# Performance work log

Hardware: AMD Instinct MI355X
Metric: run time of the kernel (lower is better)

The kernel has to match this reference:

```python
import jax, jax.numpy as jnp
import numpy as np

IN_CH = 256
OUT_CH = 256
STATE = 384
OUT_SEQ = 32
B_SZ = 8
SEQ = 512


def setup_inputs() -> dict:
    key = jax.random.key(0)
    ks = jax.random.split(key, 8)
    rmin, rmax, max_phase = 0.0, 1.0, 6.283
    u1 = jax.random.uniform(ks[0], (STATE,))
    u2 = jax.random.uniform(ks[1], (STATE,))
    # standard LRU stable-ring initialization
    nu_log = jnp.log(-0.5 * jnp.log(u1 * (rmax + rmin) * (rmax - rmin) + rmin ** 2))
    theta_log = jnp.log(max_phase * u2)
    lam_mod = jnp.exp(-jnp.exp(nu_log))
    gamma_log = jnp.log(jnp.sqrt(1.0 - lam_mod ** 2))
    B_re = jax.random.normal(ks[2], (STATE, IN_CH)) / np.sqrt(2 * IN_CH)
    B_im = jax.random.normal(ks[3], (STATE, IN_CH)) / np.sqrt(2 * IN_CH)
    C_re = jax.random.normal(ks[4], (OUT_CH, STATE)) / np.sqrt(STATE)
    C_im = jax.random.normal(ks[5], (OUT_CH, STATE)) / np.sqrt(STATE)
    D = jax.random.normal(ks[6], (OUT_CH, IN_CH)) / np.sqrt(IN_CH)
    x = jax.random.normal(ks[7], (B_SZ, SEQ, IN_CH))
    return dict(x=x, nu_log=nu_log, theta_log=theta_log, gamma_log=gamma_log,
                B_re=B_re, B_im=B_im, C_re=C_re, C_im=C_im, D=D)


def _lru(x, h_re, h_im, nu_log, theta_log, gamma_log, B_re, B_im, C_re, C_im, D):
    """One LRU pass over a full sequence. x: [B,S,C]. h_*: [B,N] initial complex state.
    Diagonal complex recurrence h_t = Lambda*h_{t-1} + gamma*(B x_t); y_t = Re(C h_t) + D x_t."""
    lam_mod = jnp.exp(-jnp.exp(nu_log))              # |Lambda| in (0,1)
    lre = lam_mod * jnp.cos(jnp.exp(theta_log))      # [N]
    lim = lam_mod * jnp.sin(jnp.exp(theta_log))
    gamma = jnp.exp(gamma_log)
    # input projection for whole sequence (complex, split into re/im)
    u_re = gamma * jnp.einsum('bsc,nc->bsn', x, B_re)  # [B,S,N]
    u_im = gamma * jnp.einsum('bsc,nc->bsn', x, B_im)

    def step(h, u):
        hre, him = h
        ur, ui = u
        nre = lre * hre - lim * him + ur
        nim = lre * him + lim * hre + ui
        return (nre, nim), (nre, nim)

    (h_re, h_im), (hs_re, hs_im) = jax.lax.scan(
        step, (h_re, h_im),
        (jnp.swapaxes(u_re, 0, 1), jnp.swapaxes(u_im, 0, 1)))  # scan over S
    hs_re = jnp.swapaxes(hs_re, 0, 1)  # [B,S,N]
    hs_im = jnp.swapaxes(hs_im, 0, 1)
    y = (jnp.einsum('bsn,on->bso', hs_re, C_re)
         - jnp.einsum('bsn,on->bso', hs_im, C_im)
         + jnp.einsum('bsc,oc->bso', x, D))
    return y, h_re, h_im


def reference(x, nu_log, theta_log, gamma_log, B_re, B_im, C_re, C_im, D):
    bsz = x.shape[0]
    h_re = jnp.zeros((bsz, STATE), x.dtype)   # state=None on first call -> zeros
    h_im = jnp.zeros((bsz, STATE), x.dtype)
    outs = []
    for _ in range(OUT_SEQ):
        x, h_re, h_im = _lru(x, h_re, h_im, nu_log, theta_log, gamma_log,
                             B_re, B_im, C_re, C_im, D)
        outs.append(x[:, -1:])
    return jnp.concatenate(outs, axis=-2)  # [B, OUT_SEQ, OUT_CH]
```

## Files before the change

### kernel.cpp

```cpp
#include <hip/hip_runtime.h>
#include <hip/hip_bf16.h>
#include <math.h>

typedef unsigned short u16;
typedef __attribute__((ext_vector_type(8))) short bf16x8;
typedef __attribute__((ext_vector_type(4))) float f32x4;
typedef __attribute__((ext_vector_type(16))) float f32x16;

#define IN_CH   256
#define STATE   384
#define OUT_SEQ 32
#define B_SZ    8
#define SEQ     512
#define M_ROWS  4096
#define NJ      768

#define PS_WB  (NJ*IN_CH)
#define PS_WC  (IN_CH*NJ)
#define PS_WD  (IN_CH*IN_CH)
#define PS_Z   ((size_t)M_ROWS*NJ)
#define PS_X   ((size_t)M_ROWS*IN_CH)

static constexpr size_t B_U   = 0;
static constexpr size_t B_Z   = B_U  + 8*(size_t)M_ROWS*IN_CH*4;
static constexpr size_t B_XA  = B_Z  + 3*(size_t)M_ROWS*NJ*2;
static constexpr size_t B_XB  = B_XA + 3*(size_t)M_ROWS*IN_CH*2;
static constexpr size_t B_WB  = B_XB + 3*(size_t)M_ROWS*IN_CH*2;
static constexpr size_t B_WC  = B_WB + 3*(size_t)PS_WB*2;
static constexpr size_t B_WD  = B_WC + 3*(size_t)PS_WC*2;
static constexpr size_t B_LAM = B_WD + 3*(size_t)PS_WD*2;
static constexpr size_t B_HC  = B_LAM + 2*768*4;

__device__ __forceinline__ u16 f2b(float v) {
    __hip_bfloat16 h = __float2bfloat16(v);
    return *(u16*)&h;
}
__device__ __forceinline__ float b2f(u16 u) {
    __hip_bfloat16 h = *(__hip_bfloat16*)&u;
    return __bfloat162float(h);
}
__device__ __forceinline__ void split3(float v, u16& a, u16& b, u16& c) {
    a = f2b(v);  float r1 = v  - b2f(a);
    b = f2b(r1); float r2 = r1 - b2f(b);
    c = f2b(r2);
}

__device__ __forceinline__ size_t a_idx(int row, int k, int NKC) {
    return ((size_t)(((row >> 5)*NKC + (k >> 5))*2 + ((k >> 4) & 1))*2 + ((k >> 3) & 1))*256
           + (size_t)(row & 31)*8 + (k & 7);
}

__device__ __forceinline__ void frag_decode(int r, int& t32, int& h, int& hi5,
                                            int& lo5, int& e) {
    t32 = r >> 10; int r2 = r & 1023;
    h = r2 >> 9;   int r3 = r2 & 511;
    hi5 = r3 >> 8; int r4 = r3 & 255;
    lo5 = r4 >> 3; e = r4 & 7;
}

__global__ void prep_lam_hc(const float* __restrict__ nu_log,
                            const float* __restrict__ th_log,
                            float* __restrict__ lam, float* __restrict__ lam16,
                            float* __restrict__ hc0) {
    int n = threadIdx.x;
    if (n < STATE) {
        float lm = expf(-expf(nu_log[n]));
        float th = expf(th_log[n]);
        float ar = lm * cosf(th), ai = lm * sinf(th);
        lam[2*n] = ar; lam[2*n+1] = ai;
        float pr = ar, pi = ai;
#pragma unroll
        for (int i = 0; i < 4; ++i) {
            float nr = pr*pr - pi*pi, ni = 2.f*pr*pi;
            pr = nr; pi = ni;
        }
        lam16[2*n] = pr; lam16[2*n+1] = pi;
    }
    for (int i = threadIdx.x; i < B_SZ*NJ; i += blockDim.x) hc0[i] = 0.f;
}

__global__ void prep_wb(const float* __restrict__ B_re, const float* __restrict__ B_im,
                        const float* __restrict__ gamma_log, u16* __restrict__ W) {
    int idx = blockIdx.x*blockDim.x + threadIdx.x;
    int c32 = idx >> 13, r = idx & 8191;
    int t32,h,hi5,lo5,e; frag_decode(r, t32,h,hi5,lo5,e);
    int j = c32*32 + lo5;
    int k = t32*32 + (2*h + hi5)*8 + e;
    int n = j >> 1;
    float g = expf(gamma_log[n]);
    float v = g * ((j & 1) ? B_im[n*IN_CH + k] : B_re[n*IN_CH + k]);
    u16 a,b,cc; split3(v,a,b,cc);
    W[idx] = a; W[idx + PS_WB] = b; W[idx + 2*PS_WB] = cc;
}

__global__ void prep_wcd(const float* __restrict__ C_re, const float* __restrict__ C_im,
                         const float* __restrict__ D,
                         u16* __restrict__ WC, u16* __restrict__ WD) {
    int idx = blockIdx.x*blockDim.x + threadIdx.x;
    if (idx < PS_WC) {
        int c32 = idx / 24576, r = idx % 24576;
        int t32,h,hi5,lo5,e; frag_decode(r, t32,h,hi5,lo5,e);
        int o = c32*32 + lo5;
        int j = t32*32 + (2*h + hi5)*8 + e;
        int n = j >> 1;
        float v = (j & 1) ? -C_im[o*STATE + n] : C_re[o*STATE + n];
        u16 a,b,c; split3(v,a,b,c);
        WC[idx] = a; WC[idx + PS_WC] = b; WC[idx + 2*PS_WC] = c;
    } else {
        int q = idx - PS_WC;
        int c32 = q >> 13, r = q & 8191;
        int t32,h,hi5,lo5,e; frag_decode(r, t32,h,hi5,lo5,e);
        int o = c32*32 + lo5;
        int c = t32*32 + (2*h + hi5)*8 + e;
        float v = D[o*IN_CH + c];
        u16 a,b,cc; split3(v,a,b,cc);
        WD[q] = a; WD[q + PS_WD] = b; WD[q + 2*PS_WD] = cc;
    }
}

__global__ void prep_x(const float* __restrict__ x,
                       u16* __restrict__ X1, u16* __restrict__ X2, u16* __restrict__ X3) {
    int idx = blockIdx.x*blockDim.x + threadIdx.x;
    int row = idx >> 8, k = idx & 255;
    u16 a,b,c; split3(x[idx],a,b,c);
    size_t o = a_idx(row, k, 8);
    X1[o] = a; X2[o] = b; X3[o] = c;
}

__device__ __constant__ const int cPI[6] = {0,0,1,0,1,2};
__device__ __constant__ const int cPJ[6] = {0,1,0,2,1,0};

struct G1P { const u16* A[3]; };

__global__ __launch_bounds__(512, 2)
void front_k(G1P ga, const u16* __restrict__ WBp, const u16* __restrict__ WDp,
             u16* __restrict__ Z1, u16* __restrict__ Z2, u16* __restrict__ Z3,
             float* __restrict__ P,
             const float* __restrict__ lam, const float* __restrict__ lam16,
             const float2* __restrict__ HcIn, float2* __restrict__ HcOut) {
    __shared__ __align__(16) float Ls[512*34];
    __shared__ float2 car[32][16];
    __shared__ float2 hp[32][16];
    const int tid = threadIdx.x, lane = tid & 63, w = tid >> 6;
    const int l15 = lane & 15, q = lane >> 4;
    const int hb = q >> 1, hi5q = q & 1;
    const int hi5 = lane >> 5, lo5 = lane & 31;

    if (blockIdx.x >= 192) {
        const int mt = blockIdx.x - 192;
        const int wr = w & 1, wc = w >> 1;
        const int m32 = mt*2 + wr;
        f32x16 acc[2];
#pragma unroll
        for (int cj = 0; cj < 2; ++cj)
#pragma unroll
            for (int i = 0; i < 16; ++i) acc[cj][i] = 0.f;

        bf16x8 av[2][3][2], bv[2][2][3][2];
        auto loadA = [&](int buf, int kc) {
#pragma unroll
            for (int p = 0; p < 3; ++p)
#pragma unroll
                for (int h = 0; h < 2; ++h)
                    av[buf][p][h] = *(const bf16x8*)(ga.A[p]
                        + ((((size_t)(m32*8 + kc)*2 + h)*2 + hi5) << 8) + lo5*8);
        };
        auto loadB = [&](int buf, int kc) {
#pragma unroll
            for (int cj = 0; cj < 2; ++cj)
#pragma unroll
                for (int p = 0; p < 3; ++p)
#pragma unroll
                    for (int h = 0; h < 2; ++h)
                        bv[buf][cj][p][h] = *(const bf16x8*)(WDp + (size_t)p*PS_WD
                            + ((((size_t)((wc*2 + cj)*8 + kc)*2 + h)*2 + hi5) << 8) + lo5*8);
        };
        loadA(0, 0); loadB(0, 0);
        loadA(1, 1); loadB(1, 1);
#pragma unroll
        for (int kc = 0; kc < 8; ++kc) {
            const int cb = kc & 1;
#pragma unroll
            for (int t6 = 0; t6 < 6; ++t6)
#pragma unroll
                for (int cj = 0; cj < 2; ++cj)
#pragma unroll
                    for (int h = 0; h < 2; ++h)
                        acc[cj] = __builtin_amdgcn_mfma_f32_32x32x16_bf16(
                            av[cb][cPI[t6]][h], bv[cb][cj][cPJ[t6]][h], acc[cj], 0, 0, 0);
            if (kc + 2 < 8) { loadA(cb, kc + 2); loadB(cb, kc + 2); }
        }
#pragma unroll
        for (int cj = 0; cj < 2; ++cj)
#pragma unroll
            for (int reg = 0; reg < 16; ++reg) {
                int row = mt*64 + wr*32 + (reg & 3) + 8*(reg >> 2) + 4*hi5;
                int col = wc*64 + cj*32 + lo5;
                P[(size_t)row*IN_CH + col] = acc[cj][reg];
            }
        return;
    }

    const int b = blockIdx.x & 7, jt = blockIdx.x >> 3;

    f32x4 acc[4][2];
#pragma unroll
    for (int i = 0; i < 4; ++i)
#pragma unroll
        for (int n16 = 0; n16 < 2; ++n16) acc[i][n16] = 0.f;

    bf16x8 av[2][4][3], bv[2][2][3];
    auto loadA = [&](int buf, int kc) {
#pragma unroll
        for (int p = 0; p < 3; ++p)
#pragma unroll
            for (int i = 0; i < 4; ++i) {
                int m16 = i*8 + w;
                int row32 = b*16 + (m16 >> 1);
                int rin = ((m16 & 1) << 4) + l15;
                av[buf][i][p] = *(const bf16x8*)(ga.A[p]
                    + ((((size_t)(row32*8 + kc)*2 + hb)*2 + hi5q) << 8) + rin*8);
            }
    };
    auto loadB = [&](int buf, int kc) {
#pragma unroll
        for (int p = 0; p < 3; ++p)
#pragma unroll
            for (int n16 = 0; n16 < 2; ++n16)
                bv[buf][n16][p] = *(const bf16x8*)(WBp + (size_t)p*PS_WB
                    + ((((size_t)(jt*8 + kc)*2 + hb)*2 + hi5q) << 8) + (n16*16 + l15)*8);
    };

    loadA(0, 0); loadB(0, 0);
    loadA(1, 1); loadB(1, 1);
#pragma unroll
    for (int kc = 0; kc < 8; ++kc) {
        const int cb = kc & 1;
#pragma unroll
        for (int t6 = 0; t6 < 6; ++t6)
#pragma unroll
            for (int i = 0; i < 4; ++i)
#pragma unroll
                for (int n16 = 0; n16 < 2; ++n16)
                    acc[i][n16] = __builtin_amdgcn_mfma_f32_16x16x32_bf16(
                        av[cb][i][cPI[t6]], bv[cb][n16][cPJ[t6]], acc[i][n16], 0, 0, 0);
        if (kc + 2 < 8) { loadA(cb, kc + 2); loadB(cb, kc + 2); }
    }

#pragma unroll
    for (int i = 0; i < 4; ++i) {
        int m16 = i*8 + w;
#pragma unroll
        for (int n16 = 0; n16 < 2; ++n16)
#pragma unroll
            for (int r = 0; r < 4; ++r) {
                int s = m16*16 + q*4 + r;
                int jl = n16*16 + l15;
                Ls[s*34 + jl] = acc[i][n16][r];
            }
    }
    __syncthreads();

    {
        int st = tid & 15, ch = tid >> 4;
        int n = jt*16 + st;
        float lre = lam[2*n], lim = lam[2*n+1];
        float hr = 0.f, hm = 0.f;
#pragma unroll
        for (int t = 0; t < 16; ++t) {
            int s = ch*16 + t;
            float2 u = *(const float2*)&Ls[s*34 + 2*st];
            float nr = fmaf(lre, hr, fmaf(-lim, hm, u.x));
            float nm = fmaf(lre, hm, fmaf( lim, hr, u.y));
            hr = nr; hm = nm;
        }
        car[ch][st] = make_float2(hr, hm);
    }
    __syncthreads();

    {
        int st2 = 2*w + hi5, ch2 = lane & 31;
        int n = jt*16 + st2;
        float2 e = car[ch2][st2];
        float Ar = lam16[2*n], Ai = lam16[2*n+1];
        float Br = e.x, Bi = e.y;
#pragma unroll
        for (int d = 1; d < 32; d <<= 1) {
            int src = (lane & 32) | ((lane - d) & 31);
            float pAr = __shfl(Ar, src), pAi = __shfl(Ai, src);
            float pBr = __shfl(Br, src), pBi = __shfl(Bi, src);
            if (ch2 >= d) {
                float nAr = Ar*pAr - Ai*pAi;
                float nAi = Ar*pAi + Ai*pAr;
                float nBr = fmaf(Ar, pBr, fmaf(-Ai, pBi, Br));
                float nBi = fmaf(Ar, pBi, fmaf( Ai, pBr, Bi));
                Ar = nAr; Ai = nAi; Br = nBr; Bi = nBi;
            }
        }
        float2 s0 = HcIn[(size_t)b*STATE + n];
        if (ch2 == 31) {
            float fr = fmaf(Ar, s0.x, fmaf(-Ai, s0.y, Br));
            float fi = fmaf(Ar, s0.y, fmaf( Ai, s0.x, Bi));
            HcOut[(size_t)b*STATE + n] = make_float2(fr, fi);
        }
        int srcp = (lane & 32) | ((lane - 1) & 31);
        float eAr = __shfl(Ar, srcp), eAi = __shfl(Ai, srcp);
        float eBr = __shfl(Br, srcp), eBi = __shfl(Bi, srcp);
        float sr, si;
        if (ch2 == 0) { sr = s0.x; si = s0.y; }
        else {
            sr = fmaf(eAr, s0.x, fmaf(-eAi, s0.y, eBr));
            si = fmaf(eAr, s0.y, fmaf( eAi, s0.x, eBi));
        }
        hp[ch2][st2] = make_float2(sr, si);
    }
    __syncthreads();

    {
        int st = tid & 15, ch = tid >> 4;
        int n = jt*16 + st;
        float lre = lam[2*n], lim = lam[2*n+1];
        float2 hh = hp[ch][st];
        int j0 = jt*32 + 2*st;
#pragma unroll
        for (int t = 0; t < 16; ++t) {
            int s = ch*16 + t;
            float2 u = *(const float2*)&Ls[s*34 + 2*st];
            float nr = fmaf(lre, hh.x, fmaf(-lim, hh.y, u.x));
            float ni = fmaf(lre, hh.y, fmaf( lim, hh.x, u.y));
            hh.x = nr; hh.y = ni;
            u16 a1,a2,a3, c1,c2,c3;
            split3(nr, a1,a2,a3);
            split3(ni, c1,c2,c3);
            size_t zo = a_idx(b*512 + s, j0, 24);
            ushort2 t2;
            t2.x = a1; t2.y = c1; *(ushort2*)(Z1 + zo) = t2;
            t2.x = a2; t2.y = c2; *(ushort2*)(Z2 + zo) = t2;
            t2.x = a3; t2.y = c3; *(ushort2*)(Z3 + zo) = t2;
        }
    }
}

struct G2P {
    const u16* Z[3]; const u16* WC; const float* P;
    u16* O1; u16* O2; u16* O3; float* outp; int iter;
};

__global__ __launch_bounds__(512, 2)
void gemm2_k(G2P g) {
    __shared__ __align__(16) float Lred[64*64];
    const int tid = threadIdx.x, lane = tid & 63, w = tid >> 6;
    const int kg = w >> 2, wq = w & 3;
    const int wr = wq & 1, wcq = wq >> 1;
    const int m0 = blockIdx.x*64, n0 = blockIdx.y*64;
    const int hi5 = lane >> 5, lo5 = lane & 31;
    const int c32 = (n0 >> 5) + wcq;
    const int m32 = blockIdx.x*2 + wr;
    const int cbase = kg*12;

    f32x16 accv;
#pragma unroll
    for (int i = 0; i < 16; ++i) accv[i] = 0.f;

    auto aptr = [&](int p, int c, int h) -> const u16* {
        return g.Z[p] + ((((size_t)(m32*24 + c)*2 + h)*2 + hi5) << 8) + lo5*8;
    };
    auto bptr = [&](int p, int c, int h) -> const u16* {
        return g.WC + (size_t)p*PS_WC
               + ((((size_t)(c32*24 + c)*2 + h)*2 + hi5) << 8) + lo5*8;
    };

    bf16x8 bwin[3][4][2];
    auto loadB = [&](int wnd, int tlo, int thi) {
#pragma unroll
        for (int p = 0; p < 3; ++p)
#pragma unroll
            for (int t = 0; t < 4; ++t) {
                if (t < tlo || t >= thi) continue;
#pragma unroll
                for (int h = 0; h < 2; ++h)
                    bwin[p][t][h] = *(const bf16x8*)bptr(p, cbase + wnd*4 + t, h);
            }
    };
    bf16x8 av[2][3][2];
    auto loadA = [&](int buf, int t) {
#pragma unroll
        for (int p = 0; p < 3; ++p)
#pragma unroll
            for (int h = 0; h < 2; ++h)
                av[buf][p][h] = *(const bf16x8*)aptr(p, cbase + t, h);
    };

    loadA(0, 0);
    loadB(0, 0, 4);
    loadA(1, 1);
#pragma unroll
    for (int t = 0; t < 12; ++t) {
        if ((t & 3) == 2 && t < 8) loadB((t >> 2) + 1, 0, 2);
        const int cb = t & 1;
        const int tw = t & 3;
#pragma unroll
        for (int t6 = 0; t6 < 6; ++t6)
            accv = __builtin_amdgcn_mfma_f32_32x32x16_bf16(
                av[cb][cPI[t6]][0], bwin[cPJ[t6]][tw][0],
                __builtin_amdgcn_mfma_f32_32x32x16_bf16(
                    av[cb][cPI[t6]][1], bwin[cPJ[t6]][tw][1], accv, 0, 0, 0),
                0, 0, 0);
        if ((t & 3) == 3 && t < 8) loadB((t >> 2) + 1, 2, 4);
        if (t + 2 < 12) loadA(cb, t + 2);
    }

    if (kg == 1) {
#pragma unroll
        for (int reg = 0; reg < 16; ++reg) {
            int rl = wr*32 + (reg & 3) + 8*(reg >> 2) + 4*hi5;
            int cl = wcq*32 + lo5;
            Lred[rl*64 + cl] = accv[reg];
        }
    }
    __syncthreads();
    if (kg == 0) {
#pragma unroll
        for (int reg = 0; reg < 16; ++reg) {
            int rl = wr*32 + (reg & 3) + 8*(reg >> 2) + 4*hi5;
            int cl = wcq*32 + lo5;
            int row = m0 + rl, col = n0 + cl;
            float v = accv[reg] + Lred[rl*64 + cl] + g.P[(size_t)row*IN_CH + col];
            u16 a,b,c; split3(v, a,b,c);
            size_t o = a_idx(row, col, 8);
            g.O1[o] = a; g.O2[o] = b; g.O3[o] = c;
            if ((row & (SEQ-1)) == SEQ-1)
                g.outp[(size_t)((row >> 9)*OUT_SEQ + g.iter)*IN_CH + col] = v;
        }
    }
}

extern "C" void kernel_launch(void* const* d_in, const int* in_sizes, int n_in,
                              void* d_out, int out_size, void* d_ws, size_t ws_size,
                              hipStream_t stream) {
    const float* x_in      = (const float*)d_in[0];
    const float* nu_log    = (const float*)d_in[1];
    const float* theta_log = (const float*)d_in[2];
    const float* gamma_log = (const float*)d_in[3];
    const float* B_re      = (const float*)d_in[4];
    const float* B_im      = (const float*)d_in[5];
    const float* C_re      = (const float*)d_in[6];
    const float* C_im      = (const float*)d_in[7];
    const float* D         = (const float*)d_in[8];
    float* out = (float*)d_out;

    char* ws = (char*)d_ws;
    float* P = (float*)(ws + B_U);
    u16* Z1 = (u16*)(ws + B_Z);
    u16* Z2 = Z1 + PS_Z;
    u16* Z3 = Z2 + PS_Z;
    u16* XA1 = (u16*)(ws + B_XA);
    u16* XA2 = XA1 + PS_X;
    u16* XA3 = XA2 + PS_X;
    u16* XB1 = (u16*)(ws + B_XB);
    u16* XB2 = XB1 + PS_X;
    u16* XB3 = XB2 + PS_X;
    u16* WB  = (u16*)(ws + B_WB);
    u16* WCt = (u16*)(ws + B_WC);
    u16* WDt = (u16*)(ws + B_WD);
    float* lam   = (float*)(ws + B_LAM);
    float* lam16 = lam + 768;
    float2* Hc0  = (float2*)(ws + B_HC);
    float2* Hc1  = Hc0 + (size_t)B_SZ*STATE;

    prep_lam_hc<<<1, 384, 0, stream>>>(nu_log, theta_log, lam, lam16, (float*)Hc0);
    prep_wb<<<PS_WB/256, 256, 0, stream>>>(B_re, B_im, gamma_log, WB);
    prep_wcd<<<(PS_WC + PS_WD)/256, 256, 0, stream>>>(C_re, C_im, D, WCt, WDt);
    prep_x<<<(M_ROWS*IN_CH)/256, 256, 0, stream>>>(x_in, XA1, XA2, XA3);

    for (int it = 0; it < OUT_SEQ; ++it) {
        u16* Xc[3]; u16* Xn[3];
        if (it & 1) { Xc[0]=XB1; Xc[1]=XB2; Xc[2]=XB3; Xn[0]=XA1; Xn[1]=XA2; Xn[2]=XA3; }
        else        { Xc[0]=XA1; Xc[1]=XA2; Xc[2]=XA3; Xn[0]=XB1; Xn[1]=XB2; Xn[2]=XB3; }
        float2* Hin  = (it & 1) ? Hc1 : Hc0;
        float2* Hout = (it & 1) ? Hc0 : Hc1;

        G1P g1;
        for (int p = 0; p < 3; ++p) g1.A[p] = Xc[p];
        front_k<<<256, 512, 0, stream>>>(
            g1, WB, WDt, Z1, Z2, Z3, P, lam, lam16, Hin, Hout);

        G2P g2;
        g2.Z[0]=Z1; g2.Z[1]=Z2; g2.Z[2]=Z3;
        g2.WC = WCt; g2.P = P;
        g2.O1 = Xn[0]; g2.O2 = Xn[1]; g2.O3 = Xn[2];
        g2.outp = out; g2.iter = it;
        gemm2_k<<<dim3(M_ROWS/64, IN_CH/64), 512, 0, stream>>>(g2);
    }
}
```

Baseline: 1.262 ms.

## Merge prep kernels, remap block order, and store local scan prefixes

The three weight and input prep kernels become one launch that uses index-range dispatch. Block indices in the front D-GEMM and in gemm2 are remapped so consecutive blocks are spread across batches and m-tiles, likely to improve cache or XCD locality. The chunked scan now writes each zero-start local prefix back into shared memory in its first pass. The second pass then reconstructs each state as lambda^t times the carried-in state plus that stored prefix, removing the serial dependency on the recurrence at the cost of extra complex multiplies.

Result: no change. 1.270 ms (+0.7%).

```diff
diff --git a/kernel.cpp b/kernel.cpp
--- a/kernel.cpp
+++ b/kernel.cpp
@@ -79,24 +79,26 @@
     for (int i = threadIdx.x; i < B_SZ*NJ; i += blockDim.x) hc0[i] = 0.f;
 }
 
-__global__ void prep_wb(const float* __restrict__ B_re, const float* __restrict__ B_im,
-                        const float* __restrict__ gamma_log, u16* __restrict__ W) {
+__global__ void prep_big(const float* __restrict__ B_re, const float* __restrict__ B_im,
+                         const float* __restrict__ gamma_log,
+                         const float* __restrict__ C_re, const float* __restrict__ C_im,
+                         const float* __restrict__ D, const float* __restrict__ x,
+                         u16* __restrict__ W, u16* __restrict__ WC, u16* __restrict__ WD,
+                         u16* __restrict__ X1, u16* __restrict__ X2, u16* __restrict__ X3) {
     int idx = blockIdx.x*blockDim.x + threadIdx.x;
-    int c32 = idx >> 13, r = idx & 8191;
-    int t32,h,hi5,lo5,e; frag_decode(r, t32,h,hi5,lo5,e);
-    int j = c32*32 + lo5;
-    int k = t32*32 + (2*h + hi5)*8 + e;
-    int n = j >> 1;
-    float g = expf(gamma_log[n]);
-    float v = g * ((j & 1) ? B_im[n*IN_CH + k] : B_re[n*IN_CH + k]);
-    u16 a,b,cc; split3(v,a,b,cc);
-    W[idx] = a; W[idx + PS_WB] = b; W[idx + 2*PS_WB] = cc;
-}
-
-__global__ void prep_wcd(const float* __restrict__ C_re, const float* __restrict__ C_im,
-                         const float* __restrict__ D,
-                         u16* __restrict__ WC, u16* __restrict__ WD) {
-    int idx = blockIdx.x*blockDim.x + threadIdx.x;
+    if (idx < PS_WB) {
+        int c32 = idx >> 13, r = idx & 8191;
+        int t32,h,hi5,lo5,e; frag_decode(r, t32,h,hi5,lo5,e);
+        int j = c32*32 + lo5;
+        int k = t32*32 + (2*h + hi5)*8 + e;
+        int n = j >> 1;
+        float g = expf(gamma_log[n]);
+        float v = g * ((j & 1) ? B_im[n*IN_CH + k] : B_re[n*IN_CH + k]);
+        u16 a,b,cc; split3(v,a,b,cc);
+        W[idx] = a; W[idx + PS_WB] = b; W[idx + 2*PS_WB] = cc;
+        return;
+    }
+    idx -= PS_WB;
     if (idx < PS_WC) {
         int c32 = idx / 24576, r = idx % 24576;
         int t32,h,hi5,lo5,e; frag_decode(r, t32,h,hi5,lo5,e);
@@ -106,25 +108,26 @@
         float v = (j & 1) ? -C_im[o*STATE + n] : C_re[o*STATE + n];
         u16 a,b,c; split3(v,a,b,c);
         WC[idx] = a; WC[idx + PS_WC] = b; WC[idx + 2*PS_WC] = c;
-    } else {
-        int q = idx - PS_WC;
-        int c32 = q >> 13, r = q & 8191;
+        return;
+    }
+    idx -= PS_WC;
+    if (idx < PS_WD) {
+        int c32 = idx >> 13, r = idx & 8191;
         int t32,h,hi5,lo5,e; frag_decode(r, t32,h,hi5,lo5,e);
         int o = c32*32 + lo5;
         int c = t32*32 + (2*h + hi5)*8 + e;
         float v = D[o*IN_CH + c];
         u16 a,b,cc; split3(v,a,b,cc);
-        WD[q] = a; WD[q + PS_WD] = b; WD[q + 2*PS_WD] = cc;
-    }
-}
-
-__global__ void prep_x(const float* __restrict__ x,
-                       u16* __restrict__ X1, u16* __restrict__ X2, u16* __restrict__ X3) {
-    int idx = blockIdx.x*blockDim.x + threadIdx.x;
-    int row = idx >> 8, k = idx & 255;
-    u16 a,b,c; split3(x[idx],a,b,c);
-    size_t o = a_idx(row, k, 8);
-    X1[o] = a; X2[o] = b; X3[o] = c;
+        WD[idx] = a; WD[idx + PS_WD] = b; WD[idx + 2*PS_WD] = cc;
+        return;
+    }
+    idx -= PS_WD;
+    {
+        int row = idx >> 8, k = idx & 255;
+        u16 a,b,c; split3(x[idx],a,b,c);
+        size_t o = a_idx(row, k, 8);
+        X1[o] = a; X2[o] = b; X3[o] = c;
+    }
 }
 
 __device__ __constant__ const int cPI[6] = {0,0,1,0,1,2};
@@ -147,7 +150,8 @@
     const int hi5 = lane >> 5, lo5 = lane & 31;
 
     if (blockIdx.x >= 192) {
-        const int mt = blockIdx.x - 192;
+        const int k0 = blockIdx.x - 192;
+        const int mt = (k0 & 7)*8 + (k0 >> 3);
         const int wr = w & 1, wc = w >> 1;
         const int m32 = mt*2 + wr;
         f32x16 acc[2];
@@ -273,6 +277,7 @@
             float nr = fmaf(lre, hr, fmaf(-lim, hm, u.x));
             float nm = fmaf(lre, hm, fmaf( lim, hr, u.y));
             hr = nr; hm = nm;
+            *(float2*)&Ls[s*34 + 2*st] = make_float2(hr, hm);
         }
         car[ch][st] = make_float2(hr, hm);
     }
@@ -321,17 +326,20 @@
         int n = jt*16 + st;
         float lre = lam[2*n], lim = lam[2*n+1];
         float2 hh = hp[ch][st];
+        float lpr = lre, lpi = lim;
         int j0 = jt*32 + 2*st;
 #pragma unroll
         for (int t = 0; t < 16; ++t) {
             int s = ch*16 + t;
-            float2 u = *(const float2*)&Ls[s*34 + 2*st];
-            float nr = fmaf(lre, hh.x, fmaf(-lim, hh.y, u.x));
-            float ni = fmaf(lre, hh.y, fmaf( lim, hh.x, u.y));
-            hh.x = nr; hh.y = ni;
+            float2 hl = *(const float2*)&Ls[s*34 + 2*st];
+            float vr = fmaf(lpr, hh.x, fmaf(-lpi, hh.y, hl.x));
+            float vi = fmaf(lpr, hh.y, fmaf( lpi, hh.x, hl.y));
+            float nlr = lpr*lre - lpi*lim;
+            float nli = lpr*lim + lpi*lre;
+            lpr = nlr; lpi = nli;
             u16 a1,a2,a3, c1,c2,c3;
-            split3(nr, a1,a2,a3);
-            split3(ni, c1,c2,c3);
+            split3(vr, a1,a2,a3);
+            split3(vi, c1,c2,c3);
             size_t zo = a_idx(b*512 + s, j0, 24);
             ushort2 t2;
             t2.x = a1; t2.y = c1; *(ushort2*)(Z1 + zo) = t2;
@@ -352,10 +360,13 @@
     const int tid = threadIdx.x, lane = tid & 63, w = tid >> 6;
     const int kg = w >> 2, wq = w & 3;
     const int wr = wq & 1, wcq = wq >> 1;
-    const int m0 = blockIdx.x*64, n0 = blockIdx.y*64;
+    const int bid = blockIdx.x;
+    const int b = bid & 7, mloc = (bid >> 3) & 7, n_t = bid >> 6;
+    const int mtile = b*8 + mloc;
+    const int m0 = mtile*64, n0 = n_t*64;
     const int hi5 = lane >> 5, lo5 = lane & 31;
-    const int c32 = (n0 >> 5) + wcq;
-    const int m32 = blockIdx.x*2 + wr;
+    const int c32 = n_t*2 + wcq;
+    const int m32 = mtile*2 + wr;
     const int cbase = kg*12;
 
     f32x16 accv;
@@ -469,9 +480,8 @@
     float2* Hc1  = Hc0 + (size_t)B_SZ*STATE;
 
     prep_lam_hc<<<1, 384, 0, stream>>>(nu_log, theta_log, lam, lam16, (float*)Hc0);
-    prep_wb<<<PS_WB/256, 256, 0, stream>>>(B_re, B_im, gamma_log, WB);
-    prep_wcd<<<(PS_WC + PS_WD)/256, 256, 0, stream>>>(C_re, C_im, D, WCt, WDt);
-    prep_x<<<(M_ROWS*IN_CH)/256, 256, 0, stream>>>(x_in, XA1, XA2, XA3);
+    prep_big<<<5888, 256, 0, stream>>>(B_re, B_im, gamma_log, C_re, C_im, D, x_in,
+                                       WB, WCt, WDt, XA1, XA2, XA3);
 
     for (int it = 0; it < OUT_SEQ; ++it) {
         u16* Xc[3]; u16* Xn[3];
@@ -490,6 +500,6 @@
         g2.WC = WCt; g2.P = P;
         g2.O1 = Xn[0]; g2.O2 = Xn[1]; g2.O3 = Xn[2];
         g2.outp = out; g2.iter = it;
-        gemm2_k<<<dim3(M_ROWS/64, IN_CH/64), 512, 0, stream>>>(g2);
-    }
-}
+        gemm2_k<<<256, 512, 0, stream>>>(g2);
+    }
+}
```
